# Performance work log

Measured on AMD Instinct MI355X. Metric: run time of the kernel, lower is better.

The kernel has to match this reference:

```python
import jax, jax.numpy as jnp
import numpy as np

HARDNESS = 5.0

def setup_inputs() -> dict:
    key = jax.random.key(0)
    k1, k2 = jax.random.split(key)
    x = jax.random.normal(k1, (64, 8, 32, 32, 16), dtype=jnp.float32)
    ref = jax.random.normal(k2, (64, 16), dtype=jnp.float32)
    return {"input": x, "ref": ref}

def reference(input, ref):
    # Squared L2 distance from every element vector (last dim) to every codeword,
    x2 = jnp.sum(input * input, axis=-1)                      # (D1,D2,D3,D4)
    r2 = jnp.sum(ref * ref, axis=-1)                          # (M,)
    cross = jnp.einsum('abcde,me->mabcd', input, ref)         # (M,D1,D2,D3,D4)
    sq_l2 = x2[None] - 2.0 * cross + r2[:, None, None, None, None]
    # Softmax over codebook axis with -hardness temperature (dim=0 in torch).
    y = jax.nn.softmax(-HARDNESS * sq_l2, axis=0)             # (M,D1,D2,D3,D4)
    # Weighted combination of codewords.
    z = jnp.einsum('mabcd,me->abcde', y, ref)                 # (D1..D5)
    return z
```

## Files before the change

### kernel.cpp

```cpp
#include <hip/hip_runtime.h>
#include <math.h>

#define CB_M 64
#define CB_D 16
#define HARD 5.0f
#define LOG2E 1.44269504088896340736f

typedef __attribute__((ext_vector_type(8))) short bf16x8;
typedef __attribute__((ext_vector_type(4))) float f32x4;
typedef __attribute__((ext_vector_type(4))) int   i32x4;

#if __has_builtin(__builtin_amdgcn_exp2f)
#define EXP2F(x) __builtin_amdgcn_exp2f(x)
#else
#define EXP2F(x) exp2f(x)
#endif

#if __has_builtin(__builtin_amdgcn_rcpf)
#define RCPF(x) __builtin_amdgcn_rcpf(x)
#else
#define RCPF(x) (1.0f / (x))
#endif

__device__ __forceinline__ ushort f2bf_rne(float f) {
    unsigned u = __float_as_uint(f);
    u += 0x7fffu + ((u >> 16) & 1u);
    return (ushort)(u >> 16);
}
__device__ __forceinline__ float bf2f(ushort h) {
    return __uint_as_float(((unsigned)h) << 16);
}
__device__ __forceinline__ int pk(float a, float b) {
    return (int)__builtin_amdgcn_perm(__float_as_uint(a), __float_as_uint(b), 0x07060302u);
}
__device__ __forceinline__ float rnd(float a) {
    return __uint_as_float(__float_as_uint(a) + 0x8000u);
}
__device__ __forceinline__ float hi_trunc(float a) {
    return __uint_as_float(__float_as_uint(a) & 0xffff0000u);
}

__global__ __launch_bounds__(256, 2) void stq_main(const float* __restrict__ x,
                                                   const float* __restrict__ ref,
                                                   float* __restrict__ out,
                                                   int ntiles) {
    __shared__ __align__(16) float  cb_bias[CB_M];
    __shared__ __align__(16) ushort cb_rs_hi[CB_M][CB_D];
    __shared__ __align__(16) ushort cb_rs_lo[CB_M][CB_D];
    __shared__ __align__(16) ushort cb_rzT_hi[CB_D][CB_M];
    __shared__ __align__(16) ushort cb_rzT_lo[CB_D][CB_M];

    const int tid = threadIdx.x;

    if (tid < CB_M) {
        const f32x4* rp = (const f32x4*)(ref + tid * CB_D);
        f32x4 q0 = rp[0], q1 = rp[1], q2 = rp[2], q3 = rp[3];
        float r[CB_D] = {q0.x,q0.y,q0.z,q0.w, q1.x,q1.y,q1.z,q1.w,
                         q2.x,q2.y,q2.z,q2.w, q3.x,q3.y,q3.z,q3.w};
        float r2 = 0.0f;
#pragma unroll
        for (int j = 0; j < CB_D; ++j) r2 += r[j] * r[j];
        cb_bias[tid] = -(HARD * LOG2E) * r2;
        const float s = 2.0f * HARD * LOG2E;
#pragma unroll
        for (int j = 0; j < CB_D; ++j) {
            float v = s * r[j];
            ushort h = f2bf_rne(v);
            cb_rs_hi[tid][j] = h;
            cb_rs_lo[tid][j] = f2bf_rne(v - bf2f(h));
            ushort zh = f2bf_rne(r[j]);
            cb_rzT_hi[j][tid] = zh;
            cb_rzT_lo[j][tid] = f2bf_rne(r[j] - bf2f(zh));
        }
    }
    __syncthreads();

    const int lane = tid & 63;
    const int wid  = tid >> 6;
    const int i = lane & 15;
    const int c = lane >> 4;

    bf16x8 A1[4], A2[4];
    f32x4  cinit[4];
    bf16x8 zfrag;
#pragma unroll
    for (int j = 0; j < 8; ++j) zfrag[j] = 0;
#pragma unroll
    for (int t = 0; t < 4; ++t) {
        const int cwa = 32 * (t >> 1) + 8 * (i >> 2) + 4 * (t & 1) + (i & 3);
        const ushort* src = (c < 2) ? &cb_rs_hi[cwa][0] : &cb_rs_lo[cwa][0];
        A1[t] = *(const bf16x8*)(src + (c & 1) * 8);
        A2[t] = (c < 2) ? A1[t] : zfrag;
#pragma unroll
        for (int r = 0; r < 4; ++r)
            cinit[t][r] = cb_bias[32 * (t >> 1) + 8 * c + 4 * (t & 1) + r];
    }
    bf16x8 BzH0 = *(const bf16x8*)&cb_rzT_hi[i][c * 8];
    bf16x8 BzH1 = *(const bf16x8*)&cb_rzT_hi[i][32 + c * 8];
    bf16x8 BzL0 = *(const bf16x8*)&cb_rzT_lo[i][c * 8];
    bf16x8 BzL1 = *(const bf16x8*)&cb_rzT_lo[i][32 + c * 8];

    const int nwaves = gridDim.x * 4;
    int tile = blockIdx.x * 4 + wid;

    f32x4 nxa, nxb;
    {
        const float* xp = x + ((size_t)tile * 16 + i) * CB_D + (c & 1) * 8;
        nxa = *(const f32x4*)xp;
        nxb = *(const f32x4*)(xp + 4);
    }

#pragma unroll 1
    for (; tile < ntiles; tile += nwaves) {
        f32x4 xa = nxa, xb = nxb;
        const int nt = tile + nwaves;
        if (nt < ntiles) {
            const float* xp = x + ((size_t)nt * 16 + i) * CB_D + (c & 1) * 8;
            nxa = *(const f32x4*)xp;
            nxb = *(const f32x4*)(xp + 4);
        }

        i32x4 B1i, B2i;
        B1i.x = pk(xa.y, xa.x); B1i.y = pk(xa.w, xa.z);
        B1i.z = pk(xb.y, xb.x); B1i.w = pk(xb.w, xb.z);
        float l0 = xa.x - hi_trunc(xa.x), l1 = xa.y - hi_trunc(xa.y);
        float l2 = xa.z - hi_trunc(xa.z), l3 = xa.w - hi_trunc(xa.w);
        float l4 = xb.x - hi_trunc(xb.x), l5 = xb.y - hi_trunc(xb.y);
        float l6 = xb.z - hi_trunc(xb.z), l7 = xb.w - hi_trunc(xb.w);
        B2i.x = pk(rnd(l1), rnd(l0)); B2i.y = pk(rnd(l3), rnd(l2));
        B2i.z = pk(rnd(l5), rnd(l4)); B2i.w = pk(rnd(l7), rnd(l6));
        bf16x8 B1 = __builtin_bit_cast(bf16x8, B1i);
        bf16x8 B2 = __builtin_bit_cast(bf16x8, B2i);

        f32x4 acc[4];
#pragma unroll
        for (int t = 0; t < 4; ++t) {
            acc[t] = __builtin_amdgcn_mfma_f32_16x16x32_bf16(A1[t], B1, cinit[t], 0, 0, 0);
            acc[t] = __builtin_amdgcn_mfma_f32_16x16x32_bf16(A2[t], B2, acc[t], 0, 0, 0);
        }

        float lmax = acc[0][0];
#pragma unroll
        for (int t = 0; t < 4; ++t)
#pragma unroll
            for (int r = 0; r < 4; ++r) lmax = fmaxf(lmax, acc[t][r]);
        lmax = fmaxf(lmax, __shfl_xor(lmax, 16, 64));
        lmax = fmaxf(lmax, __shfl_xor(lmax, 32, 64));

        float e[4][4];
        float lsum = 0.0f;
#pragma unroll
        for (int t = 0; t < 4; ++t)
#pragma unroll
            for (int r = 0; r < 4; ++r) { e[t][r] = EXP2F(acc[t][r] - lmax); lsum += e[t][r]; }
        lsum += __shfl_xor(lsum, 16, 64);
        lsum += __shfl_xor(lsum, 32, 64);
        const float inv = RCPF(lsum);

        i32x4 P1i, P2i;
        P1i.x = pk(rnd(e[0][1] * inv), rnd(e[0][0] * inv));
        P1i.y = pk(rnd(e[0][3] * inv), rnd(e[0][2] * inv));
        P1i.z = pk(rnd(e[1][1] * inv), rnd(e[1][0] * inv));
        P1i.w = pk(rnd(e[1][3] * inv), rnd(e[1][2] * inv));
        P2i.x = pk(rnd(e[2][1] * inv), rnd(e[2][0] * inv));
        P2i.y = pk(rnd(e[2][3] * inv), rnd(e[2][2] * inv));
        P2i.z = pk(rnd(e[3][1] * inv), rnd(e[3][0] * inv));
        P2i.w = pk(rnd(e[3][3] * inv), rnd(e[3][2] * inv));
        bf16x8 P1 = __builtin_bit_cast(bf16x8, P1i);
        bf16x8 P2 = __builtin_bit_cast(bf16x8, P2i);

        f32x4 z0 = {0.0f, 0.0f, 0.0f, 0.0f};
        f32x4 z1 = {0.0f, 0.0f, 0.0f, 0.0f};
        z0 = __builtin_amdgcn_mfma_f32_16x16x32_bf16(P1, BzH0, z0, 0, 0, 0);
        z1 = __builtin_amdgcn_mfma_f32_16x16x32_bf16(P1, BzL0, z1, 0, 0, 0);
        z0 = __builtin_amdgcn_mfma_f32_16x16x32_bf16(P2, BzH1, z0, 0, 0, 0);
        z1 = __builtin_amdgcn_mfma_f32_16x16x32_bf16(P2, BzL1, z1, 0, 0, 0);

        const int rowbase = tile * 16;
#pragma unroll
        for (int r = 0; r < 4; ++r)
            out[(size_t)(rowbase + 4 * c + r) * CB_D + i] = z0[r] + z1[r];
    }
}

extern "C" void kernel_launch(void* const* d_in, const int* in_sizes, int n_in,
                              void* d_out, int out_size, void* d_ws, size_t ws_size,
                              hipStream_t stream) {
    const float* x   = (const float*)d_in[0];
    const float* ref = (const float*)d_in[1];
    float* out = (float*)d_out;

    const int nvec = in_sizes[0] / CB_D;
    const int ntiles = nvec / 16;

    stq_main<<<1024, 256, 0, stream>>>(x, ref, out, ntiles);
}
```

Before: 88.74 us.

## Precompute codebook fragments in a prep kernel and launch one wave per tile pair

Result: slower. 94.52 us (+6.5%).

```diff
diff --git a/kernel.cpp b/kernel.cpp
--- a/kernel.cpp
+++ b/kernel.cpp
@@ -40,45 +40,62 @@
     return __uint_as_float(__float_as_uint(a) & 0xffff0000u);
 }
 
-__global__ __launch_bounds__(256, 2) void stq_main(const float* __restrict__ x,
-                                                   const float* __restrict__ ref,
+__global__ void stq_prep(const float* __restrict__ ref, char* __restrict__ ws) {
+    float*  bias   = (float*)(ws);
+    ushort* rs_hi  = (ushort*)(ws + 256);
+    ushort* rs_lo  = (ushort*)(ws + 2304);
+    ushort* rzT_hi = (ushort*)(ws + 4352);
+    ushort* rzT_lo = (ushort*)(ws + 6400);
+
+    int m = threadIdx.x;
+    if (m >= CB_M) return;
+    float r[CB_D];
+    float r2 = 0.0f;
+#pragma unroll
+    for (int j = 0; j < CB_D; ++j) { r[j] = ref[m * CB_D + j]; r2 += r[j] * r[j]; }
+    bias[m] = -(HARD * LOG2E) * r2;
+    const float s = 2.0f * HARD * LOG2E;
+#pragma unroll
+    for (int j = 0; j < CB_D; ++j) {
+        float v = s * r[j];
+        ushort h = f2bf_rne(v);
+        rs_hi[m * CB_D + j] = h;
+        rs_lo[m * CB_D + j] = f2bf_rne(v - bf2f(h));
+        ushort zh = f2bf_rne(r[j]);
+        rzT_hi[j * CB_M + m] = zh;
+        rzT_lo[j * CB_M + m] = f2bf_rne(r[j] - bf2f(zh));
+    }
+}
+
+#define TILES_PW 2
+__global__ __launch_bounds__(256, 4) void stq_main(const float* __restrict__ x,
+                                                   const char* __restrict__ ws,
                                                    float* __restrict__ out,
                                                    int ntiles) {
-    __shared__ __align__(16) float  cb_bias[CB_M];
-    __shared__ __align__(16) ushort cb_rs_hi[CB_M][CB_D];
-    __shared__ __align__(16) ushort cb_rs_lo[CB_M][CB_D];
-    __shared__ __align__(16) ushort cb_rzT_hi[CB_D][CB_M];
-    __shared__ __align__(16) ushort cb_rzT_lo[CB_D][CB_M];
-
-    const int tid = threadIdx.x;
-
-    if (tid < CB_M) {
-        const f32x4* rp = (const f32x4*)(ref + tid * CB_D);
-        f32x4 q0 = rp[0], q1 = rp[1], q2 = rp[2], q3 = rp[3];
-        float r[CB_D] = {q0.x,q0.y,q0.z,q0.w, q1.x,q1.y,q1.z,q1.w,
-                         q2.x,q2.y,q2.z,q2.w, q3.x,q3.y,q3.z,q3.w};
-        float r2 = 0.0f;
-#pragma unroll
-        for (int j = 0; j < CB_D; ++j) r2 += r[j] * r[j];
-        cb_bias[tid] = -(HARD * LOG2E) * r2;
-        const float s = 2.0f * HARD * LOG2E;
-#pragma unroll
-        for (int j = 0; j < CB_D; ++j) {
-            float v = s * r[j];
-            ushort h = f2bf_rne(v);
-            cb_rs_hi[tid][j] = h;
-            cb_rs_lo[tid][j] = f2bf_rne(v - bf2f(h));
-            ushort zh = f2bf_rne(r[j]);
-            cb_rzT_hi[j][tid] = zh;
-            cb_rzT_lo[j][tid] = f2bf_rne(r[j] - bf2f(zh));
-        }
-    }
-    __syncthreads();
-
-    const int lane = tid & 63;
-    const int wid  = tid >> 6;
+    const float*  bias   = (const float*)(ws);
+    const ushort* rs_hi  = (const ushort*)(ws + 256);
+    const ushort* rs_lo  = (const ushort*)(ws + 2304);
+    const ushort* rzT_hi = (const ushort*)(ws + 4352);
+    const ushort* rzT_lo = (const ushort*)(ws + 6400);
+
+    const int lane = threadIdx.x & 63;
+    const int wid  = threadIdx.x >> 6;
     const int i = lane & 15;
     const int c = lane >> 4;
+
+    const int wave_id = blockIdx.x * 4 + wid;
+    const int t0 = wave_id * TILES_PW;
+    if (t0 >= ntiles) return;
+
+    f32x4 xa0, xb0, xa1, xb1;
+    {
+        const float* xp0 = x + ((size_t)t0 * 16 + i) * CB_D + (c & 1) * 8;
+        xa0 = *(const f32x4*)xp0;
+        xb0 = *(const f32x4*)(xp0 + 4);
+        const float* xp1 = xp0 + 16 * CB_D;
+        xa1 = *(const f32x4*)xp1;
+        xb1 = *(const f32x4*)(xp1 + 4);
+    }
 
     bf16x8 A1[4], A2[4];
     f32x4  cinit[4];
@@ -88,37 +105,24 @@
 #pragma unroll
     for (int t = 0; t < 4; ++t) {
         const int cwa = 32 * (t >> 1) + 8 * (i >> 2) + 4 * (t & 1) + (i & 3);
-        const ushort* src = (c < 2) ? &cb_rs_hi[cwa][0] : &cb_rs_lo[cwa][0];
+        const ushort* src = (c < 2) ? (rs_hi + cwa * CB_D) : (rs_lo + cwa * CB_D);
         A1[t] = *(const bf16x8*)(src + (c & 1) * 8);
         A2[t] = (c < 2) ? A1[t] : zfrag;
 #pragma unroll
         for (int r = 0; r < 4; ++r)
-            cinit[t][r] = cb_bias[32 * (t >> 1) + 8 * c + 4 * (t & 1) + r];
-    }
-    bf16x8 BzH0 = *(const bf16x8*)&cb_rzT_hi[i][c * 8];
-    bf16x8 BzH1 = *(const bf16x8*)&cb_rzT_hi[i][32 + c * 8];
-    bf16x8 BzL0 = *(const bf16x8*)&cb_rzT_lo[i][c * 8];
-    bf16x8 BzL1 = *(const bf16x8*)&cb_rzT_lo[i][32 + c * 8];
-
-    const int nwaves = gridDim.x * 4;
-    int tile = blockIdx.x * 4 + wid;
-
-    f32x4 nxa, nxb;
-    {
-        const float* xp = x + ((size_t)tile * 16 + i) * CB_D + (c & 1) * 8;
-        nxa = *(const f32x4*)xp;
-        nxb = *(const f32x4*)(xp + 4);
-    }
-
-#pragma unroll 1
-    for (; tile < ntiles; tile += nwaves) {
-        f32x4 xa = nxa, xb = nxb;
-        const int nt = tile + nwaves;
-        if (nt < ntiles) {
-            const float* xp = x + ((size_t)nt * 16 + i) * CB_D + (c & 1) * 8;
-            nxa = *(const f32x4*)xp;
-            nxb = *(const f32x4*)(xp + 4);
-        }
+            cinit[t][r] = bias[32 * (t >> 1) + 8 * c + 4 * (t & 1) + r];
+    }
+    bf16x8 BzH0 = *(const bf16x8*)(rzT_hi + i * CB_M + c * 8);
+    bf16x8 BzH1 = *(const bf16x8*)(rzT_hi + i * CB_M + 32 + c * 8);
+    bf16x8 BzL0 = *(const bf16x8*)(rzT_lo + i * CB_M + c * 8);
+    bf16x8 BzL1 = *(const bf16x8*)(rzT_lo + i * CB_M + 32 + c * 8);
+
+#pragma unroll
+    for (int q = 0; q < TILES_PW; ++q) {
+        const int tile = t0 + q;
+        if (tile >= ntiles) break;
+        f32x4 xa = q ? xa1 : xa0;
+        f32x4 xb = q ? xb1 : xb0;
 
         i32x4 B1i, B2i;
         B1i.x = pk(xa.y, xa.x); B1i.y = pk(xa.w, xa.z);
@@ -189,9 +193,14 @@
     const float* x   = (const float*)d_in[0];
     const float* ref = (const float*)d_in[1];
     float* out = (float*)d_out;
+    char* ws = (char*)d_ws;
 
     const int nvec = in_sizes[0] / CB_D;
     const int ntiles = nvec / 16;
 
-    stq_main<<<1024, 256, 0, stream>>>(x, ref, out, ntiles);
-}
+    stq_prep<<<1, 64, 0, stream>>>(ref, ws);
+
+    const int waves = (ntiles + TILES_PW - 1) / TILES_PW;
+    const int blocks = (waves + 3) / 4;
+    stq_main<<<blocks, 256, 0, stream>>>(x, ws, out, ntiles);
+}
```

## Drop low-part codebook MFMAs in output GEMM, raise occupancy and grid size

Applied to the files above, without the earlier changes.

Measured after the change: 87.94 us. Within noise of the previous version (-0.9%).

```diff
diff --git a/kernel.cpp b/kernel.cpp
--- a/kernel.cpp
+++ b/kernel.cpp
@@ -40,7 +40,7 @@
     return __uint_as_float(__float_as_uint(a) & 0xffff0000u);
 }
 
-__global__ __launch_bounds__(256, 2) void stq_main(const float* __restrict__ x,
+__global__ __launch_bounds__(256, 4) void stq_main(const float* __restrict__ x,
                                                    const float* __restrict__ ref,
                                                    float* __restrict__ out,
                                                    int ntiles) {
@@ -48,7 +48,6 @@
     __shared__ __align__(16) ushort cb_rs_hi[CB_M][CB_D];
     __shared__ __align__(16) ushort cb_rs_lo[CB_M][CB_D];
     __shared__ __align__(16) ushort cb_rzT_hi[CB_D][CB_M];
-    __shared__ __align__(16) ushort cb_rzT_lo[CB_D][CB_M];
 
     const int tid = threadIdx.x;
 
@@ -68,9 +67,7 @@
             ushort h = f2bf_rne(v);
             cb_rs_hi[tid][j] = h;
             cb_rs_lo[tid][j] = f2bf_rne(v - bf2f(h));
-            ushort zh = f2bf_rne(r[j]);
-            cb_rzT_hi[j][tid] = zh;
-            cb_rzT_lo[j][tid] = f2bf_rne(r[j] - bf2f(zh));
+            cb_rzT_hi[j][tid] = f2bf_rne(r[j]);
         }
     }
     __syncthreads();
@@ -79,26 +76,21 @@
     const int wid  = tid >> 6;
     const int i = lane & 15;
     const int c = lane >> 4;
+    const bool hiquad = (c < 2);
 
-    bf16x8 A1[4], A2[4];
+    bf16x8 A1[4];
     f32x4  cinit[4];
-    bf16x8 zfrag;
-#pragma unroll
-    for (int j = 0; j < 8; ++j) zfrag[j] = 0;
 #pragma unroll
     for (int t = 0; t < 4; ++t) {
         const int cwa = 32 * (t >> 1) + 8 * (i >> 2) + 4 * (t & 1) + (i & 3);
-        const ushort* src = (c < 2) ? &cb_rs_hi[cwa][0] : &cb_rs_lo[cwa][0];
+        const ushort* src = hiquad ? &cb_rs_hi[cwa][0] : &cb_rs_lo[cwa][0];
         A1[t] = *(const bf16x8*)(src + (c & 1) * 8);
-        A2[t] = (c < 2) ? A1[t] : zfrag;
 #pragma unroll
         for (int r = 0; r < 4; ++r)
             cinit[t][r] = cb_bias[32 * (t >> 1) + 8 * c + 4 * (t & 1) + r];
     }
     bf16x8 BzH0 = *(const bf16x8*)&cb_rzT_hi[i][c * 8];
     bf16x8 BzH1 = *(const bf16x8*)&cb_rzT_hi[i][32 + c * 8];
-    bf16x8 BzL0 = *(const bf16x8*)&cb_rzT_lo[i][c * 8];
-    bf16x8 BzL1 = *(const bf16x8*)&cb_rzT_lo[i][32 + c * 8];
 
     const int nwaves = gridDim.x * 4;
     int tile = blockIdx.x * 4 + wid;
@@ -127,8 +119,10 @@
         float l2 = xa.z - hi_trunc(xa.z), l3 = xa.w - hi_trunc(xa.w);
         float l4 = xb.x - hi_trunc(xb.x), l5 = xb.y - hi_trunc(xb.y);
         float l6 = xb.z - hi_trunc(xb.z), l7 = xb.w - hi_trunc(xb.w);
-        B2i.x = pk(rnd(l1), rnd(l0)); B2i.y = pk(rnd(l3), rnd(l2));
-        B2i.z = pk(rnd(l5), rnd(l4)); B2i.w = pk(rnd(l7), rnd(l6));
+        B2i.x = hiquad ? pk(rnd(l1), rnd(l0)) : 0;
+        B2i.y = hiquad ? pk(rnd(l3), rnd(l2)) : 0;
+        B2i.z = hiquad ? pk(rnd(l5), rnd(l4)) : 0;
+        B2i.w = hiquad ? pk(rnd(l7), rnd(l6)) : 0;
         bf16x8 B1 = __builtin_bit_cast(bf16x8, B1i);
         bf16x8 B2 = __builtin_bit_cast(bf16x8, B2i);
 
@@ -136,7 +130,7 @@
 #pragma unroll
         for (int t = 0; t < 4; ++t) {
             acc[t] = __builtin_amdgcn_mfma_f32_16x16x32_bf16(A1[t], B1, cinit[t], 0, 0, 0);
-            acc[t] = __builtin_amdgcn_mfma_f32_16x16x32_bf16(A2[t], B2, acc[t], 0, 0, 0);
+            acc[t] = __builtin_amdgcn_mfma_f32_16x16x32_bf16(A1[t], B2, acc[t], 0, 0, 0);
         }
 
         float lmax = acc[0][0];
@@ -147,39 +141,38 @@
         lmax = fmaxf(lmax, __shfl_xor(lmax, 16, 64));
         lmax = fmaxf(lmax, __shfl_xor(lmax, 32, 64));
 
-        float e[4][4];
         float lsum = 0.0f;
 #pragma unroll
         for (int t = 0; t < 4; ++t)
 #pragma unroll
-            for (int r = 0; r < 4; ++r) { e[t][r] = EXP2F(acc[t][r] - lmax); lsum += e[t][r]; }
+            for (int r = 0; r < 4; ++r) {
+                acc[t][r] = EXP2F(acc[t][r] - lmax);
+                lsum += acc[t][r];
+            }
         lsum += __shfl_xor(lsum, 16, 64);
         lsum += __shfl_xor(lsum, 32, 64);
         const float inv = RCPF(lsum);
 
         i32x4 P1i, P2i;
-        P1i.x = pk(rnd(e[0][1] * inv), rnd(e[0][0] * inv));
-        P1i.y = pk(rnd(e[0][3] * inv), rnd(e[0][2] * inv));
-        P1i.z = pk(rnd(e[1][1] * inv), rnd(e[1][0] * inv));
-        P1i.w = pk(rnd(e[1][3] * inv), rnd(e[1][2] * inv));
-        P2i.x = pk(rnd(e[2][1] * inv), rnd(e[2][0] * inv));
-        P2i.y = pk(rnd(e[2][3] * inv), rnd(e[2][2] * inv));
-        P2i.z = pk(rnd(e[3][1] * inv), rnd(e[3][0] * inv));
-        P2i.w = pk(rnd(e[3][3] * inv), rnd(e[3][2] * inv));
+        P1i.x = pk(rnd(acc[0][1] * inv), rnd(acc[0][0] * inv));
+        P1i.y = pk(rnd(acc[0][3] * inv), rnd(acc[0][2] * inv));
+        P1i.z = pk(rnd(acc[1][1] * inv), rnd(acc[1][0] * inv));
+        P1i.w = pk(rnd(acc[1][3] * inv), rnd(acc[1][2] * inv));
+        P2i.x = pk(rnd(acc[2][1] * inv), rnd(acc[2][0] * inv));
+        P2i.y = pk(rnd(acc[2][3] * inv), rnd(acc[2][2] * inv));
+        P2i.z = pk(rnd(acc[3][1] * inv), rnd(acc[3][0] * inv));
+        P2i.w = pk(rnd(acc[3][3] * inv), rnd(acc[3][2] * inv));
         bf16x8 P1 = __builtin_bit_cast(bf16x8, P1i);
         bf16x8 P2 = __builtin_bit_cast(bf16x8, P2i);
 
-        f32x4 z0 = {0.0f, 0.0f, 0.0f, 0.0f};
-        f32x4 z1 = {0.0f, 0.0f, 0.0f, 0.0f};
-        z0 = __builtin_amdgcn_mfma_f32_16x16x32_bf16(P1, BzH0, z0, 0, 0, 0);
-        z1 = __builtin_amdgcn_mfma_f32_16x16x32_bf16(P1, BzL0, z1, 0, 0, 0);
-        z0 = __builtin_amdgcn_mfma_f32_16x16x32_bf16(P2, BzH1, z0, 0, 0, 0);
-        z1 = __builtin_amdgcn_mfma_f32_16x16x32_bf16(P2, BzL1, z1, 0, 0, 0);
+        f32x4 z = {0.0f, 0.0f, 0.0f, 0.0f};
+        z = __builtin_amdgcn_mfma_f32_16x16x32_bf16(P1, BzH0, z, 0, 0, 0);
+        z = __builtin_amdgcn_mfma_f32_16x16x32_bf16(P2, BzH1, z, 0, 0, 0);
 
         const int rowbase = tile * 16;
 #pragma unroll
         for (int r = 0; r < 4; ++r)
-            out[(size_t)(rowbase + 4 * c + r) * CB_D + i] = z0[r] + z1[r];
+            out[(size_t)(rowbase + 4 * c + r) * CB_D + i] = z[r];
     }
 }
 
@@ -193,5 +186,5 @@
     const int nvec = in_sizes[0] / CB_D;
     const int ntiles = nvec / 16;
 
-    stq_main<<<1024, 256, 0, stream>>>(x, ref, out, ntiles);
+    stq_main<<<2048, 256, 0, stream>>>(x, ref, out, ntiles);
 }
```
